# Kernel optimization log

Hardware: AMD Instinct MI355X
Metric: run time of the kernel (lower is better)

Reference implementation:

```python
import jax, jax.numpy as jnp
import numpy as np

GROUP, BS, CH = 16, 8192, 256


def setup_inputs() -> dict:
    key = jax.random.key(0)
    kx, kw = jax.random.split(key)
    x = jax.random.normal(kx, (GROUP, BS, CH), dtype=jnp.float32)
    # PyTorch init: uniform(-stdv, stdv), stdv = 1/sqrt(channels)
    stdv = 1.0 / np.sqrt(CH)
    weight = jax.random.uniform(kw, (GROUP, CH, CH), dtype=jnp.float32,
                                minval=-stdv, maxval=stdv)
    return {"x": x, "weight": weight}


def reference(x, weight):
    # x: (group, bs, n); weight: (group, n, channels). For each column i of
    # weight (w: (group, n)) apply Householder-style reflection sequentially:
    #   x <- x - (2 / (w^T w)) * (x @ w) w^T
    ws = jnp.moveaxis(weight, -1, 0)  # (channels, group, n)

    def step(xc, w):
        denom = jnp.sum(w * w, axis=-1)              # (group,)
        xw = jnp.einsum('gbn,gn->gb', xc, w)         # (group, bs)
        xc = xc - (2.0 / denom)[:, None, None] * xw[..., None] * w[:, None, :]
        return xc, None

    out, _ = jax.lax.scan(step, x, ws)
    return out
```

## Files before the change

### kernel.cpp

```cpp
#include <hip/hip_runtime.h>
#include <hip/hip_bf16.h>

#define GROUPS 16
#define BSZ    8192
#define CHN    256

using f32x4  = __attribute__((ext_vector_type(4))) float;
using bf16x8 = __attribute__((ext_vector_type(8))) __bf16;

static __device__ __forceinline__ unsigned short f32_bf16(float f) {
    unsigned int u = __builtin_bit_cast(unsigned int, f);
    u = (u + 0x7FFFu + ((u >> 16) & 1u)) >> 16;
    return (unsigned short)u;
}
static __device__ __forceinline__ unsigned int pack_bf16x2(float lo, float hi) {
    return (unsigned int)f32_bf16(lo) | ((unsigned int)f32_bf16(hi) << 16);
}

static __device__ __forceinline__ void gload_lds16(const void* g, void* l) {
    __builtin_amdgcn_global_load_lds(
        (const __attribute__((address_space(1))) unsigned int*)g,
        (__attribute__((address_space(3))) unsigned int*)l, 16, 0, 0);
}

__global__ __launch_bounds__(256) void compose_m(const float* __restrict__ weight,
                                                 unsigned short* __restrict__ Mt) {
    __shared__ float wbuf[16 * 260];
    __shared__ float coefbuf[16];

    const int t    = threadIdx.x;
    const int g    = blockIdx.x >> 4;
    const int r0   = (blockIdx.x & 15) * 16;
    const int lane = t & 15;
    const int rg   = (t >> 4) & 3;
    const int wave = t >> 6;
    const int r    = r0 + wave * 4 + rg;

    float4 m4[4];
#pragma unroll
    for (int j = 0; j < 4; ++j) {
        const int cb = 4 * lane + 64 * j;
        m4[j].x = (cb + 0 == r) ? 1.0f : 0.0f;
        m4[j].y = (cb + 1 == r) ? 1.0f : 0.0f;
        m4[j].z = (cb + 2 == r) ? 1.0f : 0.0f;
        m4[j].w = (cb + 3 == r) ? 1.0f : 0.0f;
    }

    const float* wg = weight + (size_t)g * CHN * CHN;
    const int e16 = t & 15;
    const int nb  = t >> 4;

    for (int iw = 0; iw < 16; ++iw) {
        const int i0 = iw * 16;
        float ld[16];
#pragma unroll
        for (int k = 0; k < 16; ++k)
            ld[k] = wg[(nb + 16 * k) * CHN + i0 + e16];
        __syncthreads();
#pragma unroll
        for (int k = 0; k < 16; ++k)
            wbuf[e16 * 260 + nb + 16 * k] = ld[k];
        __syncthreads();
        {
            const int e = t >> 4;
            float s = 0.0f;
#pragma unroll
            for (int k = 0; k < 16; ++k) {
                const float w = wbuf[e * 260 + lane + 16 * k];
                s += w * w;
            }
            s += __shfl_xor(s, 1);
            s += __shfl_xor(s, 2);
            s += __shfl_xor(s, 4);
            s += __shfl_xor(s, 8);
            if (lane == 0) coefbuf[e] = 2.0f / s;
        }
        __syncthreads();
#pragma unroll
        for (int e = 0; e < 16; ++e) {
            float4 w4[4];
#pragma unroll
            for (int j = 0; j < 4; ++j)
                w4[j] = *(const float4*)&wbuf[e * 260 + 4 * lane + 64 * j];
            float p = 0.0f;
#pragma unroll
            for (int j = 0; j < 4; ++j)
                p += m4[j].x * w4[j].x + m4[j].y * w4[j].y +
                     m4[j].z * w4[j].z + m4[j].w * w4[j].w;
            p += __shfl_xor(p, 1);
            p += __shfl_xor(p, 2);
            p += __shfl_xor(p, 4);
            p += __shfl_xor(p, 8);
            const float s = coefbuf[e] * p;
#pragma unroll
            for (int j = 0; j < 4; ++j) {
                m4[j].x -= s * w4[j].x;
                m4[j].y -= s * w4[j].y;
                m4[j].z -= s * w4[j].z;
                m4[j].w -= s * w4[j].w;
            }
        }
    }

    unsigned short* mg = Mt + (size_t)g * CHN * CHN;
#pragma unroll
    for (int j = 0; j < 4; ++j) {
        const int cb = 4 * lane + 64 * j;
        mg[(size_t)(cb + 0) * CHN + r] = f32_bf16(m4[j].x);
        mg[(size_t)(cb + 1) * CHN + r] = f32_bf16(m4[j].y);
        mg[(size_t)(cb + 2) * CHN + r] = f32_bf16(m4[j].z);
        mg[(size_t)(cb + 3) * CHN + r] = f32_bf16(m4[j].w);
    }
}

#define ABUF 2560
#define BUFSZ 6656

__global__ __launch_bounds__(512, 4) void gemm_xm(const float* __restrict__ x,
                                                  const unsigned short* __restrict__ Mt,
                                                  float* __restrict__ out) {
    __shared__ __align__(16) unsigned int lds[2 * BUFSZ];

    const int t    = threadIdx.x;
    const int g    = blockIdx.x >> 6;
    const int rb   = blockIdx.x & 63;
    const int r0   = rb * 128;
    const int l    = t & 63;
    const int wave = t >> 6;
    const int wr   = wave >> 2;
    const int wc   = wave & 3;
    const int lm   = l & 15;
    const int q    = l >> 4;

    const float*          xg = x  + ((size_t)g * BSZ + r0) * CHN;
    const unsigned short* mg = Mt +  (size_t)g * CHN * CHN;

    const int ar = t >> 3;
    const int as = t & 7;
    const int bc = (wave << 4) + ((l >> 2) & 15);
    const int bq = l & 3;

    f32x4 acc[4][4];
#pragma unroll
    for (int mi = 0; mi < 4; ++mi)
#pragma unroll
        for (int ni = 0; ni < 4; ++ni)
            acc[mi][ni] = (f32x4){0.f, 0.f, 0.f, 0.f};

    float4 sA[2][2];

    sA[0][0] = *(const float4*)&xg[(size_t)ar * CHN + 4 * as];
    sA[0][1] = *(const float4*)&xg[(size_t)(ar + 64) * CHN + 4 * as];
    {
        unsigned int* bb = lds + ABUF;
        gload_lds16(mg + (size_t)bc * CHN + 8 * bq,          &bb[wave * 256]);
        gload_lds16(mg + (size_t)(bc + 128) * CHN + 8 * bq,  &bb[(wave + 8) * 256]);
    }

#pragma unroll
    for (int kc = 0; kc < 8; ++kc) {
        const int cur = kc & 1;
        unsigned int* ab = lds + cur * BUFSZ;
        unsigned int* bb = ab + ABUF;

        {
            uint2 p0, p1;
            p0.x = pack_bf16x2(sA[cur][0].x, sA[cur][0].y);
            p0.y = pack_bf16x2(sA[cur][0].z, sA[cur][0].w);
            p1.x = pack_bf16x2(sA[cur][1].x, sA[cur][1].y);
            p1.y = pack_bf16x2(sA[cur][1].z, sA[cur][1].w);
            *(uint2*)&ab[ar * 20 + 2 * as]        = p0;
            *(uint2*)&ab[(ar + 64) * 20 + 2 * as] = p1;
        }
        __syncthreads();

        if (kc < 7) {
            const int nxt = cur ^ 1;
            const int k0  = (kc + 1) * 32;
            sA[nxt][0] = *(const float4*)&xg[(size_t)ar * CHN + k0 + 4 * as];
            sA[nxt][1] = *(const float4*)&xg[(size_t)(ar + 64) * CHN + k0 + 4 * as];
            unsigned int* bbn = lds + nxt * BUFSZ + ABUF;
            gload_lds16(mg + (size_t)bc * CHN + k0 + 8 * bq,         &bbn[wave * 256]);
            gload_lds16(mg + (size_t)(bc + 128) * CHN + k0 + 8 * bq, &bbn[(wave + 8) * 256]);
        }

        bf16x8 a[4];
#pragma unroll
        for (int mi = 0; mi < 4; ++mi) {
            const int rr = wr * 64 + mi * 16 + lm;
            a[mi] = __builtin_bit_cast(bf16x8, *(const uint4*)&ab[rr * 20 + 4 * q]);
        }
#pragma unroll
        for (int ni = 0; ni < 4; ++ni) {
            const int cc = wc * 64 + ni * 16 + lm;
            const bf16x8 b = __builtin_bit_cast(bf16x8, *(const uint4*)&bb[cc * 16 + 4 * q]);
#pragma unroll
            for (int mi = 0; mi < 4; ++mi)
                acc[mi][ni] = __builtin_amdgcn_mfma_f32_16x16x32_bf16(
                    a[mi], b, acc[mi][ni], 0, 0, 0);
        }
    }

    float* og = out + ((size_t)g * BSZ + r0) * CHN;
#pragma unroll
    for (int mi = 0; mi < 4; ++mi) {
#pragma unroll
        for (int ni = 0; ni < 4; ++ni) {
            const int col = wc * 64 + ni * 16 + lm;
#pragma unroll
            for (int reg = 0; reg < 4; ++reg) {
                const int row = wr * 64 + mi * 16 + q * 4 + reg;
                og[(size_t)row * CHN + col] = acc[mi][ni][reg];
            }
        }
    }
}

extern "C" void kernel_launch(void* const* d_in, const int* in_sizes, int n_in,
                              void* d_out, int out_size, void* d_ws, size_t ws_size,
                              hipStream_t stream) {
    const float* x = (const float*)d_in[0];
    const float* w = (const float*)d_in[1];
    float* out = (float*)d_out;
    unsigned short* Mt = (unsigned short*)d_ws;

    hipLaunchKernelGGL(compose_m, dim3(GROUPS * 16), dim3(256), 0, stream, w, Mt);
    hipLaunchKernelGGL(gemm_xm,   dim3(GROUPS * 64), dim3(512), 0, stream, x, Mt, out);
}
```

Measured before the change: 316.0 us.

## Block Householder reflections into compact-WY form and swizzle GEMM B LDS reads

After: 366.1 us. 1.16x slower.

```diff
diff --git a/kernel.cpp b/kernel.cpp
--- a/kernel.cpp
+++ b/kernel.cpp
@@ -23,10 +23,67 @@
         (__attribute__((address_space(3))) unsigned int*)l, 16, 0, 0);
 }
 
-__global__ __launch_bounds__(256) void compose_m(const float* __restrict__ weight,
-                                                 unsigned short* __restrict__ Mt) {
+static __device__ __forceinline__ float rowsum16(float x) {
+    x += __builtin_bit_cast(float, __builtin_amdgcn_mov_dpp(
+             __builtin_bit_cast(int, x), 0x128, 0xf, 0xf, true));
+    x += __builtin_bit_cast(float, __builtin_amdgcn_mov_dpp(
+             __builtin_bit_cast(int, x), 0x124, 0xf, 0xf, true));
+    x += __builtin_bit_cast(float, __builtin_amdgcn_mov_dpp(
+             __builtin_bit_cast(int, x), 0x122, 0xf, 0xf, true));
+    x += __builtin_bit_cast(float, __builtin_amdgcn_mov_dpp(
+             __builtin_bit_cast(int, x), 0x121, 0xf, 0xf, true));
+    return x;
+}
+
+__global__ __launch_bounds__(256) void prep_rw(const float* __restrict__ weight,
+                                               float* __restrict__ Rt,
+                                               float* __restrict__ wT) {
     __shared__ float wbuf[16 * 260];
-    __shared__ float coefbuf[16];
+    const int t   = threadIdx.x;
+    const int g   = blockIdx.x >> 4;
+    const int win = blockIdx.x & 15;
+    const int i0  = win * 16;
+    const float* wg = weight + (size_t)g * CHN * CHN;
+
+    const int e16 = t & 15;
+    const int nb  = t >> 4;
+#pragma unroll
+    for (int k = 0; k < 16; ++k)
+        wbuf[e16 * 260 + nb + 16 * k] = wg[(size_t)(nb + 16 * k) * CHN + i0 + e16];
+    __syncthreads();
+
+    {
+        float* wTg = wT + (size_t)g * CHN * CHN;
+        const int e  = t >> 4;
+        const int n0 = (t & 15) * 16;
+#pragma unroll
+        for (int s = 0; s < 4; ++s) {
+            const float4 v = *(const float4*)&wbuf[e * 260 + n0 + 4 * s];
+            *(float4*)&wTg[(size_t)(i0 + e) * CHN + n0 + 4 * s] = v;
+        }
+    }
+    {
+        const int e = t >> 4, f = t & 15;
+        float4 pv = {0.f, 0.f, 0.f, 0.f};
+#pragma unroll
+        for (int n4 = 0; n4 < 64; ++n4) {
+            const float4 a = *(const float4*)&wbuf[e * 260 + 4 * n4];
+            const float4 b = *(const float4*)&wbuf[f * 260 + 4 * n4];
+            pv.x += a.x * b.x; pv.y += a.y * b.y;
+            pv.z += a.z * b.z; pv.w += a.w * b.w;
+        }
+        const float s = (pv.x + pv.y) + (pv.z + pv.w);
+        float* Rtg = Rt + ((size_t)g * 16 + win) * 256;
+        if (e < f)       Rtg[f * 16 + e] = s;
+        else if (e == f) Rtg[f * 16 + e] = 2.0f / s;
+        else             Rtg[f * 16 + e] = 0.0f;
+    }
+}
+
+__global__ __launch_bounds__(256, 1) void compose_m(const float* __restrict__ wT,
+                                                    const float* __restrict__ Rt,
+                                                    unsigned short* __restrict__ Mt) {
+    __shared__ float rall[16][16][16];
 
     const int t    = threadIdx.x;
     const int g    = blockIdx.x >> 4;
@@ -36,6 +93,15 @@
     const int wave = t >> 6;
     const int r    = r0 + wave * 4 + rg;
 
+    {
+        const float* Rg = Rt + (size_t)g * 16 * 256;
+        float* rl = &rall[0][0][0];
+#pragma unroll
+        for (int k = 0; k < 16; ++k)
+            rl[t + 256 * k] = Rg[t + 256 * k];
+    }
+    __syncthreads();
+
     float4 m4[4];
 #pragma unroll
     for (int j = 0; j < 4; ++j) {
@@ -46,58 +112,49 @@
         m4[j].w = (cb + 3 == r) ? 1.0f : 0.0f;
     }
 
-    const float* wg = weight + (size_t)g * CHN * CHN;
-    const int e16 = t & 15;
-    const int nb  = t >> 4;
-
+    const float* wTg = wT + (size_t)g * CHN * CHN;
+
+#pragma unroll 1
     for (int iw = 0; iw < 16; ++iw) {
         const int i0 = iw * 16;
-        float ld[16];
-#pragma unroll
-        for (int k = 0; k < 16; ++k)
-            ld[k] = wg[(nb + 16 * k) * CHN + i0 + e16];
-        __syncthreads();
-#pragma unroll
-        for (int k = 0; k < 16; ++k)
-            wbuf[e16 * 260 + nb + 16 * k] = ld[k];
-        __syncthreads();
-        {
-            const int e = t >> 4;
-            float s = 0.0f;
-#pragma unroll
-            for (int k = 0; k < 16; ++k) {
-                const float w = wbuf[e * 260 + lane + 16 * k];
-                s += w * w;
+        float4 wc[16][4];
+#pragma unroll
+        for (int e = 0; e < 16; ++e) {
+            const float* p = wTg + (size_t)(i0 + e) * CHN + 4 * lane;
+#pragma unroll
+            for (int j = 0; j < 4; ++j)
+                wc[e][j] = *(const float4*)(p + 64 * j);
+        }
+        float s[16];
+#pragma unroll
+        for (int e = 0; e < 16; ++e) {
+            float4 pv;
+            pv.x = m4[0].x * wc[e][0].x; pv.y = m4[0].y * wc[e][0].y;
+            pv.z = m4[0].z * wc[e][0].z; pv.w = m4[0].w * wc[e][0].w;
+#pragma unroll
+            for (int j = 1; j < 4; ++j) {
+                pv.x += m4[j].x * wc[e][j].x; pv.y += m4[j].y * wc[e][j].y;
+                pv.z += m4[j].z * wc[e][j].z; pv.w += m4[j].w * wc[e][j].w;
             }
-            s += __shfl_xor(s, 1);
-            s += __shfl_xor(s, 2);
-            s += __shfl_xor(s, 4);
-            s += __shfl_xor(s, 8);
-            if (lane == 0) coefbuf[e] = 2.0f / s;
-        }
-        __syncthreads();
+            s[e] = rowsum16((pv.x + pv.y) + (pv.z + pv.w));
+        }
+        float u[16];
+#pragma unroll
+        for (int j = 0; j < 16; ++j) {
+            float acc = s[j];
+#pragma unroll
+            for (int e = 0; e < 16; ++e)
+                if (e < j) acc -= u[e] * rall[iw][j][e];
+            u[j] = acc * rall[iw][j][j];
+        }
 #pragma unroll
         for (int e = 0; e < 16; ++e) {
-            float4 w4[4];
-#pragma unroll
-            for (int j = 0; j < 4; ++j)
-                w4[j] = *(const float4*)&wbuf[e * 260 + 4 * lane + 64 * j];
-            float p = 0.0f;
-#pragma unroll
-            for (int j = 0; j < 4; ++j)
-                p += m4[j].x * w4[j].x + m4[j].y * w4[j].y +
-                     m4[j].z * w4[j].z + m4[j].w * w4[j].w;
-            p += __shfl_xor(p, 1);
-            p += __shfl_xor(p, 2);
-            p += __shfl_xor(p, 4);
-            p += __shfl_xor(p, 8);
-            const float s = coefbuf[e] * p;
 #pragma unroll
             for (int j = 0; j < 4; ++j) {
-                m4[j].x -= s * w4[j].x;
-                m4[j].y -= s * w4[j].y;
-                m4[j].z -= s * w4[j].z;
-                m4[j].w -= s * w4[j].w;
+                m4[j].x -= u[e] * wc[e][j].x;
+                m4[j].y -= u[e] * wc[e][j].y;
+                m4[j].z -= u[e] * wc[e][j].z;
+                m4[j].w -= u[e] * wc[e][j].w;
             }
         }
     }
@@ -138,7 +195,8 @@
     const int ar = t >> 3;
     const int as = t & 7;
     const int bc = (wave << 4) + ((l >> 2) & 15);
-    const int bq = l & 3;
+    const int bq = (l & 3) ^ ((l >> 3) & 3);
+    const int rq = 4 * (q ^ ((lm >> 1) & 3));
 
     f32x4 acc[4][4];
 #pragma unroll
@@ -193,7 +251,7 @@
 #pragma unroll
         for (int ni = 0; ni < 4; ++ni) {
             const int cc = wc * 64 + ni * 16 + lm;
-            const bf16x8 b = __builtin_bit_cast(bf16x8, *(const uint4*)&bb[cc * 16 + 4 * q]);
+            const bf16x8 b = __builtin_bit_cast(bf16x8, *(const uint4*)&bb[cc * 16 + rq]);
 #pragma unroll
             for (int mi = 0; mi < 4; ++mi)
                 acc[mi][ni] = __builtin_amdgcn_mfma_f32_16x16x32_bf16(
@@ -223,7 +281,10 @@
     const float* w = (const float*)d_in[1];
     float* out = (float*)d_out;
     unsigned short* Mt = (unsigned short*)d_ws;
-
-    hipLaunchKernelGGL(compose_m, dim3(GROUPS * 16), dim3(256), 0, stream, w, Mt);
+    float* Rt = (float*)((char*)d_ws + (2u << 20));
+    float* wT = (float*)((char*)d_ws + (2u << 20) + (256u << 10));
+
+    hipLaunchKernelGGL(prep_rw,   dim3(GROUPS * 16), dim3(256), 0, stream, w, Rt, wT);
+    hipLaunchKernelGGL(compose_m, dim3(GROUPS * 16), dim3(256), 0, stream, wT, Rt, Mt);
     hipLaunchKernelGGL(gemm_xm,   dim3(GROUPS * 64), dim3(512), 0, stream, x, Mt, out);
 }
```
